# Kernel optimization log

Hardware: AMD Instinct MI355X
Metric: run time of the kernel (lower is better)

## Reference

```python
import jax, jax.numpy as jnp
import numpy as np

B, S, D, H, FFN = 2, 2048, 1024, 8, 4096
DK = D // H            # head key/query dim = 128
VD = 2 * D             # double_v_dim -> v_dim = 2048
DV = VD // H           # per-head value dim = 256
SCALE_BASE = 512.0
EPS = 1e-5


def _dup_interleave(m):
    # (S, d/2) -> (S, d), each column repeated twice adjacently
    return jnp.repeat(m, 2, axis=-1)


def _rotate_every_two(x):
    x1 = x[..., 0::2]
    x2 = x[..., 1::2]
    return jnp.stack((-x2, x1), axis=-1).reshape(x.shape)


def _xpos(x, downscale):
    # x: (B,H,S,d) -- XPOS rotary with length-dependent scale
    d = x.shape[-1]
    pos = jnp.arange(x.shape[-2], dtype=jnp.float32)
    sv = (jnp.arange(0, d, 2, dtype=jnp.float32) + 0.4 * d) / (1.4 * d)  # (d/2,)
    scale = sv[None, :] ** (pos / SCALE_BASE)[:, None]                    # (S, d/2)
    half = d // 2
    inv_freq = 1.0 / (10000.0 ** (jnp.arange(half, dtype=jnp.float32) / half))
    sinusoid = pos[:, None] * inv_freq[None, :]                           # (S, d/2)
    if downscale:
        scale = 1.0 / scale
    sin = _dup_interleave(jnp.sin(sinusoid) * scale)                      # (S, d)
    cos = _dup_interleave(jnp.cos(sinusoid) * scale)
    return x * cos + _rotate_every_two(x) * sin


def _gammas(heads):
    return 1.0 - jnp.exp(jnp.linspace(np.log(1 / 32), np.log(1 / 512), heads)).astype(jnp.float32)


def _layernorm(x, w, b):
    mu = jnp.mean(x, axis=-1, keepdims=True)
    var = jnp.var(x, axis=-1, keepdims=True)
    return (x - mu) * jax.lax.rsqrt(var + EPS) * w + b


def setup_inputs() -> dict:
    key = jax.random.key(0)
    ks = jax.random.split(key, 16)
    sD = 1.0 / np.sqrt(D)
    sF = 1.0 / np.sqrt(FFN)
    return {
        "X": jax.random.normal(ks[0], (B, S, D), jnp.float32),
        "Wq": jax.random.normal(ks[1], (H, D, DK), jnp.float32) * sD,
        "Wk": jax.random.normal(ks[2], (H, D, DK), jnp.float32) * sD,
        "Wv": jax.random.normal(ks[3], (H, D, DV), jnp.float32) * sD,
        "W_G": jax.random.normal(ks[4], (D, VD), jnp.float32) * sD,
        "W_O": jax.random.normal(ks[5], (VD, D), jnp.float32) / np.sqrt(VD),
        "gn_w": jnp.ones((VD,), jnp.float32),
        "gn_b": jnp.zeros((VD,), jnp.float32),
        "ln1_w": jnp.ones((D,), jnp.float32),
        "ln1_b": jnp.zeros((D,), jnp.float32),
        "ln2_w": jnp.ones((D,), jnp.float32),
        "ln2_b": jnp.zeros((D,), jnp.float32),
        "ffn_w1": jax.random.normal(ks[6], (D, FFN), jnp.float32) * sD,
        "ffn_b1": jnp.zeros((FFN,), jnp.float32),
        "ffn_w2": jax.random.normal(ks[7], (FFN, D), jnp.float32) * sF,
        "ffn_b2": jnp.zeros((D,), jnp.float32),
    }


def _retention(Xn, Wq, Wk, Wv, W_G, W_O, gn_w, gn_b):
    # Xn: (B,S,D) pre-normalized input
    Q = jnp.einsum("bsd,hdk->bhsk", Xn, Wq)
    K = jnp.einsum("bsd,hdk->bhsk", Xn, Wk)
    V = jnp.einsum("bsd,hdv->bhsv", Xn, Wv)
    Q = _xpos(Q, downscale=False)
    K = _xpos(K, downscale=True)
    # decay matrix D[h,n,m] = gamma_h^(n-m) for n>=m else 0
    n = jnp.arange(S)[:, None]
    m = jnp.arange(S)[None, :]
    mask = (n >= m)
    exponent = jnp.where(mask, (n - m).astype(jnp.float32), 0.0)
    g = _gammas(H)
    Dmat = jnp.where(mask[None], g[:, None, None] ** exponent[None], 0.0)  # (H,S,S)
    ret = jnp.einsum("bhsk,bhtk->bhst", Q, K) * Dmat[None]
    Y = jnp.einsum("bhst,bhtv->bhsv", ret, V)                              # (B,H,S,DV)
    Y = jnp.transpose(Y, (0, 2, 1, 3))                                     # (B,S,H,DV)
    # GroupNorm(heads, v_dim) applied per token: normalize within each head chunk
    mu = jnp.mean(Y, axis=-1, keepdims=True)
    var = jnp.var(Y, axis=-1, keepdims=True)
    Y = (Y - mu) * jax.lax.rsqrt(var + EPS)
    Y = Y.reshape(B, S, VD) * gn_w + gn_b
    G = Xn @ W_G
    gated = (G * jax.nn.sigmoid(G)) * Y                                     # swish gate
    return gated @ W_O


def reference(X, Wq, Wk, Wv, W_G, W_O, gn_w, gn_b, ln1_w, ln1_b, ln2_w, ln2_b,
              ffn_w1, ffn_b1, ffn_w2, ffn_b2):
    X = _retention(_layernorm(X, ln1_w, ln1_b), Wq, Wk, Wv, W_G, W_O, gn_w, gn_b) + X
    h = _layernorm(X, ln2_w, ln2_b)
    h = jax.nn.gelu(h @ ffn_w1 + ffn_b1, approximate=False) @ ffn_w2 + ffn_b2
    return h + X
```

## Files before the change

kernel.cpp:

```cpp
#include <hip/hip_runtime.h>
#include <hip/hip_bf16.h>

typedef unsigned short u16;
typedef unsigned int   u32;
typedef short short8 __attribute__((ext_vector_type(8)));
typedef float f32x4  __attribute__((ext_vector_type(4)));

__device__ __forceinline__ float b2f(u16 u) { return __uint_as_float(((u32)u) << 16); }
__device__ __forceinline__ u16 f2b(float f) {
    u32 u = __float_as_uint(f);
    u += 0x7FFF + ((u >> 16) & 1);
    return (u16)(u >> 16);
}
__device__ __forceinline__ float gelu_fast(float v) {
    float a = v * (2.302118f + 0.102953f * v * v);
    a = fminf(a, 120.f);
    float e = exp2f(a);
    return v * e / (1.f + e);
}

typedef const unsigned int __attribute__((address_space(1)))* gas1;
typedef unsigned int __attribute__((address_space(3)))* las3;
__device__ __forceinline__ void async_ld16(const void* g, const void* l) {
    __builtin_amdgcn_global_load_lds((gas1)(unsigned long long)g,
                                     (las3)(unsigned int)(unsigned long long)l,
                                     16, 0, 0);
}

__device__ __forceinline__ void wtrans_body(const float* __restrict__ W, u16* __restrict__ Wt,
                                            int K, int N, int bx, int by, int bz) {
    __shared__ u16 tile[32][36];
    const int k0 = bx * 32, n0 = by * 32;
    const float* Wz = W + (long)bz * K * N;
    u16* Wtz = Wt + (long)bz * K * N;
    const int t = threadIdx.x;
    const int r = t >> 3, c = (t & 7) * 4;
    float4 v = *(const float4*)(Wz + (long)(k0 + r) * N + n0 + c);
    tile[r][c+0] = f2b(v.x); tile[r][c+1] = f2b(v.y);
    tile[r][c+2] = f2b(v.z); tile[r][c+3] = f2b(v.w);
    __syncthreads();
    uint2 pk;
    pk.x = (u32)tile[c+0][r] | ((u32)tile[c+1][r] << 16);
    pk.y = (u32)tile[c+2][r] | ((u32)tile[c+3][r] << 16);
    *(uint2*)(Wtz + (long)(n0 + r) * K + k0 + c) = pk;
}

__device__ __forceinline__ void xtab_body(float4* __restrict__ tab, int blk) {
    int idx = blk * 256 + threadIdx.x;
    int j = idx & 63, s = idx >> 6;
    float sv = (2.f * j + 51.2f) / 179.2f;
    float scale = exp2f(log2f(sv) * ((float)s * (1.f / 512.f)));
    float inv_freq = exp2f((float)j * (-13.287712379549449f / 64.f));
    float ang = (float)s * inv_freq;
    float sn = sinf(ang), cs = cosf(ang);
    tab[idx] = make_float4(cs * scale, sn * scale, cs / scale, sn / scale);
}

__device__ __forceinline__ void ln_body(const float* __restrict__ X,
                                        const float* __restrict__ w,
                                        const float* __restrict__ bb,
                                        u16* __restrict__ out, long row) {
    const int t = threadIdx.x;
    float4 p = ((const float4*)(X + row * 1024))[t];
    float x[4] = { p.x, p.y, p.z, p.w };
    float s = x[0]+x[1]+x[2]+x[3];
    float q = x[0]*x[0]+x[1]*x[1]+x[2]*x[2]+x[3]*x[3];
#pragma unroll
    for (int o = 32; o > 0; o >>= 1) { s += __shfl_down(s, o, 64); q += __shfl_down(q, o, 64); }
    __shared__ float aS[4], aQ[4];
    if ((t & 63) == 0) { aS[t >> 6] = s; aQ[t >> 6] = q; }
    __syncthreads();
    s = aS[0]+aS[1]+aS[2]+aS[3];
    q = aQ[0]+aQ[1]+aQ[2]+aQ[3];
    float mean = s * (1.f/1024.f);
    float var  = q * (1.f/1024.f) - mean*mean;
    float rstd = rsqrtf(var + 1e-5f);
    float4 wv = ((const float4*)w)[t];
    float4 bv = ((const float4*)bb)[t];
    uint2 r;
    r.x = (u32)f2b((x[0]-mean)*rstd*wv.x + bv.x) | ((u32)f2b((x[1]-mean)*rstd*wv.y + bv.y) << 16);
    r.y = (u32)f2b((x[2]-mean)*rstd*wv.z + bv.z) | ((u32)f2b((x[3]-mean)*rstd*wv.w + bv.w) << 16);
    ((uint2*)(out + row * 1024))[t] = r;
}

__global__ __launch_bounds__(256) void prep_k(
    const float* __restrict__ Wq, const float* __restrict__ Wk,
    const float* __restrict__ Wv, const float* __restrict__ WG,
    const float* __restrict__ WO, const float* __restrict__ fw1,
    const float* __restrict__ fw2, const float* __restrict__ X,
    const float* __restrict__ ln1w, const float* __restrict__ ln1b,
    u16* __restrict__ WT, u16* __restrict__ WOT,
    u16* __restrict__ fw1T, u16* __restrict__ fw2T,
    float4* __restrict__ xtab, u16* __restrict__ Xn) {
    const int id = blockIdx.x;
    if (id < 16384) {
        const float* W; u16* Wt; int K, N, bx, by, bz = 0;
        if (id < 1024)       { W=Wq;  Wt=WT;           K=1024; N=128;  int l=id;       bx=l&31;  by=(l>>5)&3; bz=l>>7; }
        else if (id < 2048)  { W=Wk;  Wt=WT+1048576;   K=1024; N=128;  int l=id-1024;  bx=l&31;  by=(l>>5)&3; bz=l>>7; }
        else if (id < 4096)  { W=Wv;  Wt=WT+2097152;   K=1024; N=256;  int l=id-2048;  bx=l&31;  by=(l>>5)&7; bz=l>>8; }
        else if (id < 6144)  { W=WG;  Wt=WT+4194304;   K=1024; N=2048; int l=id-4096;  bx=l&31;  by=l>>5; }
        else if (id < 8192)  { W=WO;  Wt=WOT;          K=2048; N=1024; int l=id-6144;  bx=l&63;  by=l>>6; }
        else if (id < 12288) { W=fw1; Wt=fw1T;         K=1024; N=4096; int l=id-8192;  bx=l&31;  by=l>>5; }
        else                 { W=fw2; Wt=fw2T;         K=4096; N=1024; int l=id-12288; bx=l&127; by=l>>7; }
        wtrans_body(W, Wt, K, N, bx, by, bz);
    } else if (id < 16896) {
        xtab_body(xtab, id - 16384);
    } else {
        ln_body(X, ln1w, ln1b, Xn, id - 16896);
    }
}

__global__ __launch_bounds__(256) void ln2_combine(const float* __restrict__ P,
                                                   const float* __restrict__ X,
                                                   const float* __restrict__ w,
                                                   const float* __restrict__ bb,
                                                   float* __restrict__ X2,
                                                   u16* __restrict__ hb) {
    const long row = blockIdx.x;
    const int t = threadIdx.x;
    const float* p = P + row * 3072;
    float4 a = ((const float4*)p)[t];
    float4 c = ((const float4*)(p + 1024))[t];
    float4 xr = ((const float4*)(X + row * 1024))[t];
    float x[4] = { a.x+c.x+xr.x, a.y+c.y+xr.y, a.z+c.z+xr.z, a.w+c.w+xr.w };
    ((float4*)(X2 + row * 1024))[t] = make_float4(x[0], x[1], x[2], x[3]);
    float s = x[0]+x[1]+x[2]+x[3];
    float q = x[0]*x[0]+x[1]*x[1]+x[2]*x[2]+x[3]*x[3];
#pragma unroll
    for (int o = 32; o > 0; o >>= 1) { s += __shfl_down(s, o, 64); q += __shfl_down(q, o, 64); }
    __shared__ float aS[4], aQ[4];
    if ((t & 63) == 0) { aS[t >> 6] = s; aQ[t >> 6] = q; }
    __syncthreads();
    s = aS[0]+aS[1]+aS[2]+aS[3];
    q = aQ[0]+aQ[1]+aQ[2]+aQ[3];
    float mean = s * (1.f/1024.f);
    float var  = q * (1.f/1024.f) - mean*mean;
    float rstd = rsqrtf(var + 1e-5f);
    float4 wv = ((const float4*)w)[t];
    float4 bv = ((const float4*)bb)[t];
    uint2 r;
    r.x = (u32)f2b((x[0]-mean)*rstd*wv.x + bv.x) | ((u32)f2b((x[1]-mean)*rstd*wv.y + bv.y) << 16);
    r.y = (u32)f2b((x[2]-mean)*rstd*wv.z + bv.z) | ((u32)f2b((x[3]-mean)*rstd*wv.w + bv.w) << 16);
    ((uint2*)(hb + row * 1024))[t] = r;
}

__global__ __launch_bounds__(256) void ffn2_combine(const float* __restrict__ P,
                                                    const float* __restrict__ b2,
                                                    const float* __restrict__ X2,
                                                    float* __restrict__ out) {
    const long row = blockIdx.x;
    const int t = threadIdx.x;
    float4 p0 = ((const float4*)(P + row * 1024))[t];
    float4 p1 = ((const float4*)(P + 16777216 + row * 1024))[t];
    float4 x2 = ((const float4*)(X2 + row * 1024))[t];
    float4 bv = ((const float4*)b2)[t];
    ((float4*)(out + row * 1024))[t] = make_float4(
        p0.x + p1.x + x2.x + bv.x, p0.y + p1.y + x2.y + bv.y,
        p0.z + p1.z + x2.z + bv.z, p0.w + p1.w + x2.w + bv.w);
}

enum { EPI_GELU_BIAS = 2, EPI_QKVG = 4 };

template<int EPI, int PANELS>
__global__ __launch_bounds__(256) void mgemm(
    const u16* __restrict__ A, const u16* __restrict__ Bt, u16* __restrict__ Cv,
    int K, int aStride, long cStride,
    const float* __restrict__ bias, u16* __restrict__ Vt) {
    __shared__ __align__(16) u16 As[PANELS * 4096];
    __shared__ __align__(16) u16 Bs[PANELS * 4096];
    const int pid = blockIdx.x;
    const int mb = pid & 31;
    const int nb = pid >> 5;
    const int t = threadIdx.x;
    const int row0 = mb * 128, col0 = nb * 128;
    const int wave = t >> 6, lane = t & 63;
    const int wm = wave >> 1, wn = wave & 1;
    const int quad = lane >> 4, l16 = lane & 15;
    const u16* Ag = A + (long)(row0 + (t >> 2)) * aStride + ((t & 3) * 8);
    const u16* Bg = Bt + (long)(col0 + (t >> 2)) * K + ((t & 3) * 8);
    const long aj = (long)64 * aStride;
    const long bj = (long)64 * K;
    const u32 lo = __builtin_amdgcn_readfirstlane((u32)(wave * 1024));

    f32x4 acc[4][4];
#pragma unroll
    for (int i = 0; i < 4; i++)
#pragma unroll
        for (int j = 0; j < 4; j++) acc[i][j] = (f32x4){0.f, 0.f, 0.f, 0.f};

    for (int k0 = 0; k0 < K; k0 += PANELS * 32) {
#pragma unroll
        for (int h = 0; h < PANELS; h++) {
            const u16* Agh = Ag + k0 + h * 32;
            const u16* Bgh = Bg + k0 + h * 32;
            async_ld16(Agh,      (const char*)As + h*8192 + lo);
            async_ld16(Agh + aj, (const char*)As + h*8192 + 4096 + lo);
            async_ld16(Bgh,      (const char*)Bs + h*8192 + lo);
            async_ld16(Bgh + bj, (const char*)Bs + h*8192 + 4096 + lo);
        }
        __syncthreads();
#pragma unroll
        for (int h = 0; h < PANELS; h++) {
            short8 af[4], bf[4];
#pragma unroll
            for (int mt = 0; mt < 4; mt++)
                af[mt] = *(const short8*)(As + h*4096 + (wm*64 + mt*16 + l16) * 32 + quad*8);
#pragma unroll
            for (int nt = 0; nt < 4; nt++)
                bf[nt] = *(const short8*)(Bs + h*4096 + (wn*64 + nt*16 + l16) * 32 + quad*8);
#pragma unroll
            for (int mt = 0; mt < 4; mt++)
#pragma unroll
                for (int nt = 0; nt < 4; nt++)
                    acc[mt][nt] = __builtin_amdgcn_mfma_f32_16x16x32_bf16(af[mt], bf[nt], acc[mt][nt], 0, 0, 0);
        }
        __syncthreads();
    }

    if constexpr (EPI == EPI_QKVG) {
        if (col0 >= 2048 && col0 < 4096) {
            const int bq = row0 >> 11;
            const int sb = (row0 & 2047) + wm*64 + quad*4;
#pragma unroll
            for (int mt = 0; mt < 4; mt++) {
#pragma unroll
                for (int nt = 0; nt < 4; nt++) {
                    int vc = (col0 - 2048) + wn*64 + nt*16 + l16;
                    u16* dst = Vt + ((long)((bq << 3) + (vc >> 8)) * 256 + (vc & 255)) * 2048
                                  + sb + mt*16;
                    uint2 pk;
                    pk.x = (u32)f2b(acc[mt][nt][0]) | ((u32)f2b(acc[mt][nt][1]) << 16);
                    pk.y = (u32)f2b(acc[mt][nt][2]) | ((u32)f2b(acc[mt][nt][3]) << 16);
                    *(uint2*)dst = pk;
                }
            }
            return;
        }
    }

#pragma unroll
    for (int mt = 0; mt < 4; mt++) {
#pragma unroll
        for (int reg = 0; reg < 4; reg++) {
            int r = row0 + wm*64 + mt*16 + quad*4 + reg;
#pragma unroll
            for (int nt = 0; nt < 4; nt++) {
                int c = col0 + wn*64 + nt*16 + l16;
                float v = acc[mt][nt][reg];
                if constexpr (EPI == EPI_GELU_BIAS) {
                    v = gelu_fast(v + bias[c]);
                } else if constexpr (EPI == EPI_QKVG) {
                    if (c < 2048) {
                        int j = (c & 127) >> 1;
                        float4 tb = ((const float4*)bias)[((r & 2047) << 6) + j];
                        float cs = (c < 1024) ? tb.x : tb.z;
                        float sn = (c < 1024) ? tb.y : tb.w;
                        float partner = __shfl_xor(v, 1, 64);
                        v = v * cs + ((c & 1) ? partner : -partner) * sn;
                    }
                }
                Cv[(long)r * cStride + c] = f2b(v);
            }
        }
    }
}

__global__ __launch_bounds__(256) void mgemm_sk(
    const u16* __restrict__ A, const u16* __restrict__ Bt, float* __restrict__ P,
    int K, int kHalf, int aStride, long pRowStride, long sliceOff) {
    __shared__ __align__(16) u16 As[2 * 4096];
    __shared__ __align__(16) u16 Bs[2 * 4096];
    const int pid = blockIdx.x;
    const int mb = pid & 31;
    const int nb = (pid & 255) >> 5;
    const int slice = pid >> 8;
    const int t = threadIdx.x;
    const int row0 = mb * 128, col0 = nb * 128;
    const int wave = t >> 6, lane = t & 63;
    const int wm = wave >> 1, wn = wave & 1;
    const int quad = lane >> 4, l16 = lane & 15;
    const u16* Ag = A + (long)(row0 + (t >> 2)) * aStride + ((t & 3) * 8);
    const u16* Bg = Bt + (long)(col0 + (t >> 2)) * K + ((t & 3) * 8);
    const long aj = (long)64 * aStride;
    const long bj = (long)64 * K;
    const u32 lo = __builtin_amdgcn_readfirstlane((u32)(wave * 1024));

    f32x4 acc[4][4];
#pragma unroll
    for (int i = 0; i < 4; i++)
#pragma unroll
        for (int j = 0; j < 4; j++) acc[i][j] = (f32x4){0.f, 0.f, 0.f, 0.f};

    const int kBeg = slice * kHalf, kEnd = kBeg + kHalf;
    for (int k0 = kBeg; k0 < kEnd; k0 += 64) {
#pragma unroll
        for (int h = 0; h < 2; h++) {
            const u16* Agh = Ag + k0 + h * 32;
            const u16* Bgh = Bg + k0 + h * 32;
            async_ld16(Agh,      (const char*)As + h*8192 + lo);
            async_ld16(Agh + aj, (const char*)As + h*8192 + 4096 + lo);
            async_ld16(Bgh,      (const char*)Bs + h*8192 + lo);
            async_ld16(Bgh + bj, (const char*)Bs + h*8192 + 4096 + lo);
        }
        __syncthreads();
#pragma unroll
        for (int h = 0; h < 2; h++) {
            short8 af[4], bf[4];
#pragma unroll
            for (int mt = 0; mt < 4; mt++)
                af[mt] = *(const short8*)(As + h*4096 + (wm*64 + mt*16 + l16) * 32 + quad*8);
#pragma unroll
            for (int nt = 0; nt < 4; nt++)
                bf[nt] = *(const short8*)(Bs + h*4096 + (wn*64 + nt*16 + l16) * 32 + quad*8);
#pragma unroll
            for (int mt = 0; mt < 4; mt++)
#pragma unroll
                for (int nt = 0; nt < 4; nt++)
                    acc[mt][nt] = __builtin_amdgcn_mfma_f32_16x16x32_bf16(af[mt], bf[nt], acc[mt][nt], 0, 0, 0);
        }
        __syncthreads();
    }

    float* Pb = P + slice * sliceOff;
#pragma unroll
    for (int mt = 0; mt < 4; mt++) {
#pragma unroll
        for (int reg = 0; reg < 4; reg++) {
            int r = row0 + wm*64 + mt*16 + quad*4 + reg;
#pragma unroll
            for (int nt = 0; nt < 4; nt++) {
                int c = col0 + wn*64 + nt*16 + l16;
                Pb[(long)r * pRowStride + c] = acc[mt][nt][reg];
            }
        }
    }
}

__global__ __launch_bounds__(256) void retention_mfma(
    u16* __restrict__ QKVG, const u16* __restrict__ Vt,
    const float* __restrict__ gnw, const float* __restrict__ gnb) {
    __shared__ __align__(16) u16 Qs[4][64][32];
    __shared__ __align__(16) u16 Ks[2][4][32][32];
    __shared__ __align__(16) u16 Vs[2][256][32];
    __shared__ u16 Ss[64][40];
    const int id = blockIdx.x;
    const int halfg = id >> 8, r5 = id & 255;
    const int bh = r5 >> 4, i16 = r5 & 15;
    const int tile = halfg ? i16 : 31 - i16;
    const int b = bh >> 3, h = bh & 7;
    const int t = threadIdx.x;
    const int wave = t >> 6, lane = t & 63, quad = lane >> 4, l16 = lane & 15;
    const u32 lo = __builtin_amdgcn_readfirstlane((u32)(wave * 1024));
    const u16* Qbase = QKVG + (long)b * 2048 * 6144 + h * 128;
    const u16* Kbase = Qbase + 1024;
    const u16* Vbase = Vt + (long)(b * 8 + h) * 256 * 2048;
    u16* Gseg = QKVG + (long)b * 2048 * 6144 + 4096 + h * 256;

    float g = 1.f - expf(-3.4657359027997265f + (-0.3960841031771116f) * (float)h);
    float log2g = log2f(g);
    const float gi16 = exp2f(log2g * -16.f);
    const float gi32 = gi16 * gi16;
    const float gf[4] = {1.f, g, g*g, g*g*g};
    const int srow0 = tile*64 + wave*16 + quad*4;
    float drun = exp2f(log2g * (float)(srow0 - l16));

    auto issueKV = [&](int jt, int buf) {
#pragma unroll
        for (int i = 0; i < 2; i++) {
            int c = t + i * 256;
            int ks = c >> 7, row = (c >> 2) & 31, cb = c & 3;
            async_ld16(Kbase + (long)(jt*32 + row) * 6144 + ks*32 + cb*8,
                       (const char*)Ks + buf*8192 + i*4096 + lo);
        }
#pragma unroll
        for (int i = 0; i < 4; i++) {
            int c = t + i * 256;
            int row = c >> 2, cb = c & 3;
            async_ld16(Vbase + (long)row * 2048 + jt*32 + cb*8,
                       (const char*)Vs + buf*16384 + i*4096 + lo);
        }
    };

#pragma unroll
    for (int i = 0; i < 4; i++) {
        int c = t + i * 256;
        int ks = c >> 8, row = (c >> 2) & 63, cb = c & 3;
        async_ld16(Qbase + (long)(tile*64 + row) * 6144 + ks*32 + cb*8,
                   (const char*)Qs + i*4096 + lo);
    }
    issueKV(0, 0);

    float gw[16], gbv[16];
#pragma unroll
    for (int nt = 0; nt < 16; nt++) {
        gw[nt]  = gnw[h*256 + nt*16 + l16];
        gbv[nt] = gnb[h*256 + nt*16 + l16];
    }
    f32x4 oacc[16];
#pragma unroll
    for (int nt = 0; nt < 16; nt++) oacc[nt] = (f32x4){0.f, 0.f, 0.f, 0.f};
    __syncthreads();

    const int njt = 2 * tile + 2;
    for (int jt = 0; jt < njt; jt++) {
        const int cur = jt & 1;
        if (jt + 1 < njt) issueKV(jt + 1, cur ^ 1);
        f32x4 s0 = (f32x4){0.f,0.f,0.f,0.f}, s1 = (f32x4){0.f,0.f,0.f,0.f};
#pragma unroll
        for (int ks = 0; ks < 4; ks++) {
            short8 aq = *(const short8*)&Qs[ks][wave*16 + l16][quad*8];
            short8 b0 = *(const short8*)&Ks[cur][ks][l16][quad*8];
            short8 b1 = *(const short8*)&Ks[cur][ks][16 + l16][quad*8];
            s0 = __builtin_amdgcn_mfma_f32_16x16x32_bf16(aq, b0, s0, 0, 0, 0);
            s1 = __builtin_amdgcn_mfma_f32_16x16x32_bf16(aq, b1, s1, 0, 0, 0);
        }
#pragma unroll
        for (int reg = 0; reg < 4; reg++) {
            int srow = srow0 + reg;
            int tc0 = jt*32 + l16, tc1 = tc0 + 16;
            float dbase = drun * gf[reg];
            float d0 = (srow >= tc0) ? dbase : 0.f;
            float d1 = (srow >= tc1) ? dbase * gi16 : 0.f;
            Ss[wave*16 + quad*4 + reg][l16]      = f2b(s0[reg] * d0);
            Ss[wave*16 + quad*4 + reg][16 + l16] = f2b(s1[reg] * d1);
        }
        drun *= gi32;
        short8 as = *(const short8*)&Ss[wave*16 + l16][quad*8];
#pragma unroll
        for (int nt = 0; nt < 16; nt++) {
            short8 bv = *(const short8*)&Vs[cur][nt*16 + l16][quad*8];
            oacc[nt] = __builtin_amdgcn_mfma_f32_16x16x32_bf16(as, bv, oacc[nt], 0, 0, 0);
        }
        __syncthreads();
    }

#pragma unroll
    for (int reg = 0; reg < 4; reg++) {
        float s = 0.f, q = 0.f;
#pragma unroll
        for (int nt = 0; nt < 16; nt++) { float v = oacc[nt][reg]; s += v; q += v*v; }
#pragma unroll
        for (int m = 1; m < 16; m <<= 1) { s += __shfl_xor(s, m, 16); q += __shfl_xor(q, m, 16); }
        float mean = s * (1.f/256.f);
        float var  = q * (1.f/256.f) - mean*mean;
        float rstd = rsqrtf(var + 1e-5f);
        int srow = srow0 + reg;
        u16* grow = Gseg + (long)srow * 6144;
#pragma unroll
        for (int nt = 0; nt < 16; nt++) {
            float gval = b2f(grow[nt*16 + l16]);
            float y = (oacc[nt][reg] - mean) * rstd * gw[nt] + gbv[nt];
            float sg = gval / (1.f + exp2f(-1.4426950408889634f * gval));
            grow[nt*16 + l16] = f2b(sg * y);
        }
    }
}

extern "C" void kernel_launch(void* const* d_in, const int* in_sizes, int n_in,
                              void* d_out, int out_size, void* d_ws, size_t ws_size,
                              hipStream_t stream) {
    (void)in_sizes; (void)n_in; (void)out_size; (void)ws_size;
    const float* X    = (const float*)d_in[0];
    const float* Wq   = (const float*)d_in[1];
    const float* Wk   = (const float*)d_in[2];
    const float* Wv   = (const float*)d_in[3];
    const float* WG   = (const float*)d_in[4];
    const float* WO   = (const float*)d_in[5];
    const float* gnw  = (const float*)d_in[6];
    const float* gnb  = (const float*)d_in[7];
    const float* ln1w = (const float*)d_in[8];
    const float* ln1b = (const float*)d_in[9];
    const float* ln2w = (const float*)d_in[10];
    const float* ln2b = (const float*)d_in[11];
    const float* fw1  = (const float*)d_in[12];
    const float* fb1  = (const float*)d_in[13];
    const float* fw2  = (const float*)d_in[14];
    const float* fb2  = (const float*)d_in[15];

    constexpr int D = 1024, FFN = 4096;
    constexpr int M = 4096;
    constexpr long MB = 1048576;

    char* ws = (char*)d_ws;
    u16* WT   = (u16*)(ws + 0*MB);
    u16* WOT  = (u16*)(ws + 12*MB);
    u16* fw1T = (u16*)(ws + 16*MB);
    u16* fw2T = (u16*)(ws + 24*MB);
    u16*   QKVG = (u16*)(ws + 32*MB);
    u16*   Xn   = (u16*)(ws + 80*MB);
    float4* xtab= (float4*)(ws + 88*MB);
    u16*   Vt   = (u16*)(ws + 90*MB);
    float* X2   = (float*)(ws + 80*MB);
    u16*   hb   = (u16*)(ws + 0*MB);
    u16*   mid  = (u16*)(ws + 32*MB);
    float* PF   = (float*)(ws + 0*MB);

    prep_k<<<20992, 256, 0, stream>>>(Wq, Wk, Wv, WG, WO, fw1, fw2, X, ln1w, ln1b,
                                      WT, WOT, fw1T, fw2T, xtab, Xn);
    mgemm<EPI_QKVG, 2><<<1536, 256, 0, stream>>>(
        Xn, WT, QKVG, D, D, 6144, (const float*)xtab, Vt);
    retention_mfma<<<512, 256, 0, stream>>>(QKVG, Vt, gnw, gnb);
    mgemm_sk<<<512, 256, 0, stream>>>(
        QKVG + 4096, WOT, (float*)QKVG, 2048, 1024, 6144, 3072, 1024);
    ln2_combine<<<M, 256, 0, stream>>>((const float*)QKVG, X, ln2w, ln2b, X2, hb);
    mgemm<EPI_GELU_BIAS, 2><<<1024, 256, 0, stream>>>(
        hb, fw1T, mid, D, D, FFN, fb1, nullptr);
    mgemm_sk<<<512, 256, 0, stream>>>(
        mid, fw2T, PF, 4096, 2048, 4096, 1024, 16777216);
    ffn2_combine<<<M, 256, 0, stream>>>(PF, fb2, X2, (float*)d_out);
}
```

Measured before the change: 449.2 us.

## Replace 128x128 GEMM with double-buffered 256x256 tile, 512-thread pipelined kernel

Replaces the QKVG and FFN1 GEMM kernel with a 256x256-tile, 8-wave version that double-buffers LDS and issues the next K-tile's async loads while the current tile's MFMAs run. Blocks are remapped across groups of 8 with a swizzle, and s_setprio raises priority around the MFMA bursts. The larger tile raises data reuse per LDS load, but it uses 128KB of LDS and leaves fewer blocks (384 and 256), which risks poorer occupancy and wave-quantization tail effects on the device.

```diff
diff --git a/kernel.cpp b/kernel.cpp
--- a/kernel.cpp
+++ b/kernel.cpp
@@ -161,76 +161,97 @@
 
 enum { EPI_GELU_BIAS = 2, EPI_QKVG = 4 };
 
-template<int EPI, int PANELS>
-__global__ __launch_bounds__(256) void mgemm(
+template<int EPI>
+__global__ __launch_bounds__(512) void mgemm256(
     const u16* __restrict__ A, const u16* __restrict__ Bt, u16* __restrict__ Cv,
     int K, int aStride, long cStride,
     const float* __restrict__ bias, u16* __restrict__ Vt) {
-    __shared__ __align__(16) u16 As[PANELS * 4096];
-    __shared__ __align__(16) u16 Bs[PANELS * 4096];
-    const int pid = blockIdx.x;
-    const int mb = pid & 31;
-    const int nb = pid >> 5;
-    const int t = threadIdx.x;
-    const int row0 = mb * 128, col0 = nb * 128;
+    __shared__ __align__(16) u16 As[2][16384];
+    __shared__ __align__(16) u16 Bs[2][16384];
+    const int cpx = gridDim.x >> 3;
+    const int bid = blockIdx.x;
+    const int pid = (bid & 7) * cpx + (bid >> 3);
+    const int mb = pid & 15;
+    const int nb = pid >> 4;
+    const int t = threadIdx.x;
     const int wave = t >> 6, lane = t & 63;
-    const int wm = wave >> 1, wn = wave & 1;
+    const int wm = wave >> 2, wn = wave & 3;
     const int quad = lane >> 4, l16 = lane & 15;
-    const u16* Ag = A + (long)(row0 + (t >> 2)) * aStride + ((t & 3) * 8);
-    const u16* Bg = Bt + (long)(col0 + (t >> 2)) * K + ((t & 3) * 8);
-    const long aj = (long)64 * aStride;
-    const long bj = (long)64 * K;
+    const int row0 = mb * 256, col0 = nb * 256;
+    const u16* aBase = A + (long)(row0 + (t >> 3)) * aStride + (t & 7) * 8;
+    const u16* bBase = Bt + (long)(col0 + (t >> 3)) * K + (t & 7) * 8;
     const u32 lo = __builtin_amdgcn_readfirstlane((u32)(wave * 1024));
 
-    f32x4 acc[4][4];
-#pragma unroll
-    for (int i = 0; i < 4; i++)
+    f32x4 acc[8][4];
+#pragma unroll
+    for (int i = 0; i < 8; i++)
 #pragma unroll
         for (int j = 0; j < 4; j++) acc[i][j] = (f32x4){0.f, 0.f, 0.f, 0.f};
 
-    for (int k0 = 0; k0 < K; k0 += PANELS * 32) {
-#pragma unroll
-        for (int h = 0; h < PANELS; h++) {
-            const u16* Agh = Ag + k0 + h * 32;
-            const u16* Bgh = Bg + k0 + h * 32;
-            async_ld16(Agh,      (const char*)As + h*8192 + lo);
-            async_ld16(Agh + aj, (const char*)As + h*8192 + 4096 + lo);
-            async_ld16(Bgh,      (const char*)Bs + h*8192 + lo);
-            async_ld16(Bgh + bj, (const char*)Bs + h*8192 + 4096 + lo);
-        }
-        __syncthreads();
-#pragma unroll
-        for (int h = 0; h < PANELS; h++) {
-            short8 af[4], bf[4];
-#pragma unroll
-            for (int mt = 0; mt < 4; mt++)
-                af[mt] = *(const short8*)(As + h*4096 + (wm*64 + mt*16 + l16) * 32 + quad*8);
-#pragma unroll
-            for (int nt = 0; nt < 4; nt++)
-                bf[nt] = *(const short8*)(Bs + h*4096 + (wn*64 + nt*16 + l16) * 32 + quad*8);
-#pragma unroll
-            for (int mt = 0; mt < 4; mt++)
-#pragma unroll
-                for (int nt = 0; nt < 4; nt++)
-                    acc[mt][nt] = __builtin_amdgcn_mfma_f32_16x16x32_bf16(af[mt], bf[nt], acc[mt][nt], 0, 0, 0);
-        }
-        __syncthreads();
+    auto stage = [&](int tt, int bb, int hf) {
+        const long koff = (long)tt * 64;
+#pragma unroll
+        for (int r = hf * 2; r < hf * 2 + 2; r++) {
+            async_ld16(aBase + (long)(r * 64) * aStride + koff,
+                       (const char*)&As[bb][0] + r * 8192 + lo);
+            async_ld16(bBase + (long)(r * 64) * K + koff,
+                       (const char*)&Bs[bb][0] + r * 8192 + lo);
+        }
+    };
+
+    stage(0, 0, 0); stage(0, 0, 1);
+    asm volatile("s_waitcnt vmcnt(0)" ::: "memory");
+    __builtin_amdgcn_s_barrier();
+
+    const int nT = K >> 6;
+    for (int tt = 0; tt < nT; tt++) {
+        const int b = tt & 1;
+        const u16* Asb = &As[b][0];
+        const u16* Bsb = &Bs[b][0];
+        short8 bf[4][2];
+#pragma unroll
+        for (int nt2 = 0; nt2 < 4; nt2++)
+#pragma unroll
+            for (int kh = 0; kh < 2; kh++)
+                bf[nt2][kh] = *(const short8*)(Bsb + (wn*64 + nt2*16 + l16) * 64 + kh*32 + quad*8);
+#pragma unroll
+        for (int p = 0; p < 4; p++) {
+            if (p < 2 && tt + 1 < nT) stage(tt + 1, b ^ 1, p);
+            short8 af[2][2];
+#pragma unroll
+            for (int i = 0; i < 2; i++)
+#pragma unroll
+                for (int kh = 0; kh < 2; kh++)
+                    af[i][kh] = *(const short8*)(Asb + (wm*128 + (p*2+i)*16 + l16) * 64 + kh*32 + quad*8);
+            __builtin_amdgcn_s_setprio(1);
+#pragma unroll
+            for (int i = 0; i < 2; i++)
+#pragma unroll
+                for (int nt2 = 0; nt2 < 4; nt2++)
+#pragma unroll
+                    for (int kh = 0; kh < 2; kh++)
+                        acc[p*2+i][nt2] = __builtin_amdgcn_mfma_f32_16x16x32_bf16(
+                            af[i][kh], bf[nt2][kh], acc[p*2+i][nt2], 0, 0, 0);
+            __builtin_amdgcn_s_setprio(0);
+            if (p == 3) asm volatile("s_waitcnt vmcnt(0)" ::: "memory");
+            __builtin_amdgcn_s_barrier();
+        }
     }
 
     if constexpr (EPI == EPI_QKVG) {
         if (col0 >= 2048 && col0 < 4096) {
             const int bq = row0 >> 11;
-            const int sb = (row0 & 2047) + wm*64 + quad*4;
-#pragma unroll
-            for (int mt = 0; mt < 4; mt++) {
-#pragma unroll
-                for (int nt = 0; nt < 4; nt++) {
-                    int vc = (col0 - 2048) + wn*64 + nt*16 + l16;
+            const int sb = (row0 & 2047) + wm*128 + quad*4;
+#pragma unroll
+            for (int mt = 0; mt < 8; mt++) {
+#pragma unroll
+                for (int nt2 = 0; nt2 < 4; nt2++) {
+                    int vc = (col0 - 2048) + wn*64 + nt2*16 + l16;
                     u16* dst = Vt + ((long)((bq << 3) + (vc >> 8)) * 256 + (vc & 255)) * 2048
                                   + sb + mt*16;
                     uint2 pk;
-                    pk.x = (u32)f2b(acc[mt][nt][0]) | ((u32)f2b(acc[mt][nt][1]) << 16);
-                    pk.y = (u32)f2b(acc[mt][nt][2]) | ((u32)f2b(acc[mt][nt][3]) << 16);
+                    pk.x = (u32)f2b(acc[mt][nt2][0]) | ((u32)f2b(acc[mt][nt2][1]) << 16);
+                    pk.y = (u32)f2b(acc[mt][nt2][2]) | ((u32)f2b(acc[mt][nt2][3]) << 16);
                     *(uint2*)dst = pk;
                 }
             }
@@ -239,14 +260,14 @@
     }
 
 #pragma unroll
-    for (int mt = 0; mt < 4; mt++) {
+    for (int mt = 0; mt < 8; mt++) {
 #pragma unroll
         for (int reg = 0; reg < 4; reg++) {
-            int r = row0 + wm*64 + mt*16 + quad*4 + reg;
-#pragma unroll
-            for (int nt = 0; nt < 4; nt++) {
-                int c = col0 + wn*64 + nt*16 + l16;
-                float v = acc[mt][nt][reg];
+            int r = row0 + wm*128 + mt*16 + quad*4 + reg;
+#pragma unroll
+            for (int nt2 = 0; nt2 < 4; nt2++) {
+                int c = col0 + wn*64 + nt2*16 + l16;
+                float v = acc[mt][nt2][reg];
                 if constexpr (EPI == EPI_GELU_BIAS) {
                     v = gelu_fast(v + bias[c]);
                 } else if constexpr (EPI == EPI_QKVG) {
@@ -497,13 +518,13 @@
 
     prep_k<<<20992, 256, 0, stream>>>(Wq, Wk, Wv, WG, WO, fw1, fw2, X, ln1w, ln1b,
                                       WT, WOT, fw1T, fw2T, xtab, Xn);
-    mgemm<EPI_QKVG, 2><<<1536, 256, 0, stream>>>(
+    mgemm256<EPI_QKVG><<<384, 512, 0, stream>>>(
         Xn, WT, QKVG, D, D, 6144, (const float*)xtab, Vt);
     retention_mfma<<<512, 256, 0, stream>>>(QKVG, Vt, gnw, gnb);
     mgemm_sk<<<512, 256, 0, stream>>>(
         QKVG + 4096, WOT, (float*)QKVG, 2048, 1024, 6144, 3072, 1024);
     ln2_combine<<<M, 256, 0, stream>>>((const float*)QKVG, X, ln2w, ln2b, X2, hb);
-    mgemm<EPI_GELU_BIAS, 2><<<1024, 256, 0, stream>>>(
+    mgemm256<EPI_GELU_BIAS><<<256, 512, 0, stream>>>(
         hb, fw1T, mid, D, D, FFN, fb1, nullptr);
     mgemm_sk<<<512, 256, 0, stream>>>(
         mid, fw2T, PF, 4096, 2048, 4096, 1024, 16777216);
```

Result: slower. 510.3 us (+13.6%).
